# Performance work log

Measured on AMD Instinct MI355X. Metric: run time of the kernel, lower is better.

The kernel has to match this reference:

```python
import jax, jax.numpy as jnp
import numpy as np

B, L, D, K = 32, 4096, 1024, 64


def setup_inputs() -> dict:
    key = jax.random.key(0)
    k1, k2, k3, k4, k5 = jax.random.split(key, 5)
    feats = jax.random.normal(k1, (B, L, D), dtype=jnp.float32)
    assign_w = jax.random.normal(k2, (K, D), dtype=jnp.float32) * (1.0 / np.sqrt(D))
    assign_b = jax.random.normal(k3, (K,), dtype=jnp.float32) * 0.01
    centroids = jax.random.uniform(k4, (K, D), dtype=jnp.float32)
    # ensure at least one valid token per batch row (softmax over L stays finite)
    lens = jax.random.randint(k5, (B,), L // 2, L + 1, dtype=jnp.int32)
    return {"feats": feats, "lens": lens, "assign_w": assign_w,
            "assign_b": assign_b, "centroids": centroids}


def reference(feats, lens, assign_w, assign_b, centroids):
    # feats: (B,L,D); lens: (B,) int; assign_w: (K,D); assign_b: (K,); centroids: (K,D)
    Bq, Lq, Dq = feats.shape
    # padding mask; torch code slices to max(lens) first, but masked positions
    # contribute zero weight after softmax, so keeping full L is equivalent.
    mask = jnp.arange(Lq)[None, :] < lens[:, None]            # (B,L)
    logits = jnp.einsum('bld,kd->blk', feats, assign_w) + assign_b  # (B,L,K)
    logits = jnp.where(mask[:, :, None], logits, -jnp.inf)
    a = jax.nn.softmax(logits, axis=1)                         # softmax over L
    # (a[:,:,:,None] * (feats[:,:,None,:] - centroids)).sum(1) without
    # materializing the (B,L,K,D) residual tensor:
    s = a.sum(axis=1)                                          # (B,K), == 1 analytically
    vlad = jnp.einsum('blk,bld->bkd', a, feats) - s[..., None] * centroids[None]  # (B,K,D)
    out = vlad.min(axis=1)                                     # min over clusters -> (B,D)
    norm = jnp.maximum(jnp.linalg.norm(out, axis=-1, keepdims=True), 1e-12)
    return out / norm
```

## Files before the change

kernel.cpp:

```cpp
#include <hip/hip_runtime.h>
#include <math.h>

#define NB 32
#define NL 4096
#define ND 1024
#define NK 64
#define DTILE 128
#define S_SPLIT 4

typedef __bf16 bf16_t;
typedef __bf16 bf16x8 __attribute__((ext_vector_type(8)));
typedef __bf16 bf16x4 __attribute__((ext_vector_type(4)));
typedef float f32x4_t __attribute__((ext_vector_type(4)));

__global__ __launch_bounds__(256) void k_convw(const float* __restrict__ W,
                                               bf16_t* __restrict__ Wb) {
    const int i = (blockIdx.x * 256 + threadIdx.x) * 4;
    const float4 v = *(const float4*)(W + i);
    bf16x4 o;
    o[0] = (bf16_t)v.x; o[1] = (bf16_t)v.y; o[2] = (bf16_t)v.z; o[3] = (bf16_t)v.w;
    *(bf16x4*)(Wb + i) = o;
}

__global__ __launch_bounds__(256, 2) void k_logits(const float* __restrict__ feats,
                                                   const bf16_t* __restrict__ Wb,
                                                   const float* __restrict__ bias,
                                                   const int* __restrict__ lens,
                                                   float* __restrict__ logitsT,
                                                   float* __restrict__ pmax,
                                                   float* __restrict__ psum) {
    const int bid = blockIdx.x;
    const int b = bid >> 4;
    const int chunk = bid & 15;
    const int l0 = chunk << 8;
    const int len = lens[b];
    if (l0 >= len) return;
    const int t = threadIdx.x;
    const int w = t >> 6;
    const int lane = t & 63;
    const int lr = lane & 15;
    const int oct = lane >> 4;
    const int lw = l0 + w * 64;
    const float* fp = feats + ((size_t)b * NL + lw + lr) * ND + oct * 8;

    f32x4_t acc[4][4];
#pragma unroll
    for (int m = 0; m < 4; ++m)
#pragma unroll
        for (int j = 0; j < 4; ++j) acc[m][j] = (f32x4_t){0.f, 0.f, 0.f, 0.f};

#pragma unroll 2
    for (int kk = 0; kk < 32; ++kk) {
        const int d = kk * 32;
        bf16x8 af[4];
#pragma unroll
        for (int mt = 0; mt < 4; ++mt) {
            const float4 a0 = *(const float4*)(fp + (size_t)mt * 16 * ND + d);
            const float4 a1 = *(const float4*)(fp + (size_t)mt * 16 * ND + d + 4);
            af[mt][0] = (bf16_t)a0.x; af[mt][1] = (bf16_t)a0.y;
            af[mt][2] = (bf16_t)a0.z; af[mt][3] = (bf16_t)a0.w;
            af[mt][4] = (bf16_t)a1.x; af[mt][5] = (bf16_t)a1.y;
            af[mt][6] = (bf16_t)a1.z; af[mt][7] = (bf16_t)a1.w;
        }
#pragma unroll
        for (int j = 0; j < 4; ++j) {
            const bf16x8 bf = *(const bf16x8*)(Wb + (size_t)(j * 16 + lr) * ND + d + oct * 8);
#pragma unroll
            for (int mt = 0; mt < 4; ++mt)
                acc[mt][j] = __builtin_amdgcn_mfma_f32_16x16x32_bf16(af[mt], bf, acc[mt][j], 0, 0, 0);
        }
    }
    float vals[4][4][4];
#pragma unroll
    for (int mt = 0; mt < 4; ++mt)
#pragma unroll
        for (int j = 0; j < 4; ++j) {
            const int k = j * 16 + lr;
            const float bs = bias[k];
#pragma unroll
            for (int r = 0; r < 4; ++r) vals[mt][j][r] = acc[mt][j][r] + bs;
            const int lb = lw + mt * 16 + oct * 4;
            float4 st = make_float4(vals[mt][j][0], vals[mt][j][1], vals[mt][j][2], vals[mt][j][3]);
            *(float4*)(logitsT + ((size_t)b * NK + k) * NL + lb) = st;
        }
    __shared__ float red[64][17];
    __shared__ float bm[64];
    const int slot = w * 4 + oct;
#pragma unroll
    for (int j = 0; j < 4; ++j) {
        float vm = -1e30f;
#pragma unroll
        for (int mt = 0; mt < 4; ++mt) {
            const int lbase = lw + mt * 16 + oct * 4;
#pragma unroll
            for (int r = 0; r < 4; ++r)
                if (lbase + r < len) vm = fmaxf(vm, vals[mt][j][r]);
        }
        red[j * 16 + lr][slot] = vm;
    }
    __syncthreads();
    if (t < 64) {
        float m = -1e30f;
#pragma unroll
        for (int q = 0; q < 16; ++q) m = fmaxf(m, red[t][q]);
        bm[t] = m;
    }
    __syncthreads();
#pragma unroll
    for (int j = 0; j < 4; ++j) {
        const float mk = bm[j * 16 + lr];
        float sj = 0.f;
#pragma unroll
        for (int mt = 0; mt < 4; ++mt) {
            const int lbase = lw + mt * 16 + oct * 4;
#pragma unroll
            for (int r = 0; r < 4; ++r)
                if (lbase + r < len) sj += __expf(vals[mt][j][r] - mk);
        }
        red[j * 16 + lr][slot] = sj;
    }
    __syncthreads();
    if (t < 64) {
        float ssum = 0.f;
#pragma unroll
        for (int q = 0; q < 16; ++q) ssum += red[t][q];
        pmax[((size_t)b * 16 + chunk) * 64 + t] = bm[t];
        psum[((size_t)b * 16 + chunk) * 64 + t] = ssum;
    }
}

__global__ void k_sm2(const float* __restrict__ pmax, const float* __restrict__ psum,
                      const int* __restrict__ lens,
                      float* __restrict__ mbuf2) {
    const int b = blockIdx.x;
    const int k = threadIdx.x;
    const int nc = (lens[b] + 255) >> 8;
    float m = -1e30f;
    for (int c = 0; c < nc; ++c) m = fmaxf(m, pmax[((size_t)b * 16 + c) * 64 + k]);
    float s = 0.f;
    for (int c = 0; c < nc; ++c)
        s += psum[((size_t)b * 16 + c) * 64 + k] * __expf(pmax[((size_t)b * 16 + c) * 64 + k] - m);
    mbuf2[b * 64 + k] = m + logf(s);
}

__global__ __launch_bounds__(256, 3) void k_aggregate(const float* __restrict__ feats,
                                                      const float* __restrict__ logitsT,
                                                      const int* __restrict__ lens,
                                                      const float* __restrict__ mbuf2,
                                                      float* __restrict__ pO) {
    const int bid = blockIdx.x;
    const int s  = bid & 3;
    const int dc = (bid >> 2) & 7;
    const int b  = bid >> 5;
    const int d0 = dc * DTILE;
    const int t = threadIdx.x;
    const int kh = (t >> 6) & 1;
    const int dh = t >> 7;
    const int lane = t & 63;
    const int lr = lane & 15;
    const int oct = lane >> 4;
    const int len = lens[b];
    const int nT = (len + 63) >> 6;
    const int t0 = (nT * s) >> 2;
    const int t1 = (nT * (s + 1)) >> 2;

    __shared__ char fH[16 * 1024];

    const int kk0 = kh * 32 + lr;
    const float ms0 = mbuf2[b * 64 + kk0];
    const float ms1 = mbuf2[b * 64 + kk0 + 16];
    const float* lg0 = logitsT + ((size_t)b * NK + kk0) * NL;
    const float* lg1 = lg0 + (size_t)16 * NL;

    const int c4 = (t & 31) * 4;
    const int lf0 = (t >> 5) * 4;

    f32x4_t acc[2][4];
#pragma unroll
    for (int m = 0; m < 2; ++m)
#pragma unroll
        for (int n = 0; n < 4; ++n) acc[m][n] = (f32x4_t){0.f, 0.f, 0.f, 0.f};

    float4 pf[2][4];

#define LOADF(tile_)                                                                     \
    {                                                                                    \
        const int lb_ = (tile_) * 64;                                                    \
        _Pragma("unroll")                                                                \
        for (int p_ = 0; p_ < 2; ++p_) {                                                 \
            _Pragma("unroll")                                                            \
            for (int i_ = 0; i_ < 4; ++i_)                                               \
                pf[p_][i_] = *(const float4*)(feats +                                    \
                    ((size_t)b * NL + lb_ + p_ * 32 + lf0 + i_) * ND + d0 + c4);         \
        }                                                                                \
    }

    if (t0 < t1) LOADF(t0);

    for (int tile = t0; tile < t1; ++tile) {
        const int l0 = tile * 64;
        bf16x8 afH[2][2], afL[2][2];
#pragma unroll
        for (int mt = 0; mt < 2; ++mt) {
            const float* lg = mt ? lg1 : lg0;
            const float msk = mt ? ms1 : ms0;
            float4 g[4];
            g[0] = *(const float4*)(lg + l0 + oct * 8);
            g[1] = *(const float4*)(lg + l0 + oct * 8 + 4);
            g[2] = *(const float4*)(lg + l0 + 32 + oct * 8);
            g[3] = *(const float4*)(lg + l0 + 32 + oct * 8 + 4);
#pragma unroll
            for (int ks = 0; ks < 2; ++ks) {
#pragma unroll
                for (int h = 0; h < 2; ++h) {
                    const float4 v = g[ks * 2 + h];
                    const int lbase = l0 + ks * 32 + oct * 8 + h * 4;
                    float av[4];
                    av[0] = (lbase + 0 < len) ? __expf(v.x - msk) : 0.f;
                    av[1] = (lbase + 1 < len) ? __expf(v.y - msk) : 0.f;
                    av[2] = (lbase + 2 < len) ? __expf(v.z - msk) : 0.f;
                    av[3] = (lbase + 3 < len) ? __expf(v.w - msk) : 0.f;
#pragma unroll
                    for (int c = 0; c < 4; ++c) {
                        const bf16_t hi = (bf16_t)av[c];
                        afH[mt][ks][h * 4 + c] = hi;
                        afL[mt][ks][h * 4 + c] = (bf16_t)(av[c] - (float)hi);
                    }
                }
            }
        }
        __syncthreads();
#pragma unroll
        for (int p = 0; p < 2; ++p) {
            const int l4 = p * 32 + lf0;
#pragma unroll
            for (int j = 0; j < 4; ++j) {
                const int d = c4 + j;
                bf16x4 hi;
                hi[0] = (bf16_t)(&pf[p][0].x)[j];
                hi[1] = (bf16_t)(&pf[p][1].x)[j];
                hi[2] = (bf16_t)(&pf[p][2].x)[j];
                hi[3] = (bf16_t)(&pf[p][3].x)[j];
                const int chunk = (l4 >> 3) ^ ((d ^ (d >> 3)) & 7);
                const int off = d * 128 + (chunk << 4) + (l4 & 7) * 2;
                *(bf16x4*)(fH + off) = hi;
            }
        }
        if (tile + 1 < t1) LOADF(tile + 1);
        __syncthreads();
#pragma unroll
        for (int ks = 0; ks < 2; ++ks) {
            const int cbase = ks * 4 + oct;
            bf16x8 bfv[4];
#pragma unroll
            for (int n = 0; n < 4; ++n) {
                const int d = dh * 64 + n * 16 + lr;
                const int foff = d * 128 + ((cbase ^ ((d ^ (d >> 3)) & 7)) << 4);
                bfv[n] = *(const bf16x8*)(fH + foff);
            }
#pragma unroll
            for (int mt = 0; mt < 2; ++mt)
#pragma unroll
                for (int n = 0; n < 4; ++n) {
                    acc[mt][n] = __builtin_amdgcn_mfma_f32_16x16x32_bf16(afH[mt][ks], bfv[n], acc[mt][n], 0, 0, 0);
                    acc[mt][n] = __builtin_amdgcn_mfma_f32_16x16x32_bf16(afL[mt][ks], bfv[n], acc[mt][n], 0, 0, 0);
                }
        }
    }
#undef LOADF
    float* po = pO + ((size_t)((b * 8 + dc) * S_SPLIT + s)) * (NK * DTILE);
#pragma unroll
    for (int mt = 0; mt < 2; ++mt)
#pragma unroll
        for (int n = 0; n < 4; ++n) {
#pragma unroll
            for (int r = 0; r < 4; ++r) {
                const int k = kh * 32 + mt * 16 + oct * 4 + r;
                po[k * DTILE + dh * 64 + n * 16 + lr] = acc[mt][n][r];
            }
        }
}

__global__ __launch_bounds__(128) void k_combine(const float* __restrict__ pO,
                                                 const float* __restrict__ centroids,
                                                 float* __restrict__ outun) {
    const int b = blockIdx.x >> 3;
    const int d = (blockIdx.x & 7) * 128 + threadIdx.x;
    const int dc = d >> 7;
    const int dl = d & 127;
    const float* base = pO + ((size_t)(b * 8 + dc)) * S_SPLIT * NK * DTILE;
    float mn = 1e30f;
    for (int k = 0; k < NK; ++k) {
        float v = 0.f;
#pragma unroll
        for (int s = 0; s < S_SPLIT; ++s) v += base[(size_t)(s * NK + k) * DTILE + dl];
        v -= centroids[(size_t)k * ND + d];
        mn = fminf(mn, v);
    }
    outun[(size_t)b * ND + d] = mn;
}

__global__ __launch_bounds__(256) void k_norm(const float* __restrict__ outun,
                                              float* __restrict__ out) {
    const int b = blockIdx.x;
    const int t = threadIdx.x;
    float ss = 0.f;
    for (int d = t; d < ND; d += 256) {
        const float v = outun[(size_t)b * ND + d];
        ss += v * v;
    }
#pragma unroll
    for (int off = 32; off > 0; off >>= 1) ss += __shfl_down(ss, off);
    __shared__ float red[4];
    if ((t & 63) == 0) red[t >> 6] = ss;
    __syncthreads();
    const float tot = red[0] + red[1] + red[2] + red[3];
    const float inv = 1.0f / fmaxf(sqrtf(tot), 1e-12f);
    for (int d = t; d < ND; d += 256) out[(size_t)b * ND + d] = outun[(size_t)b * ND + d] * inv;
}

extern "C" void kernel_launch(void* const* d_in, const int* in_sizes, int n_in,
                              void* d_out, int out_size, void* d_ws, size_t ws_size,
                              hipStream_t stream) {
    const float* feats     = (const float*)d_in[0];
    const int*   lens      = (const int*)d_in[1];
    const float* W         = (const float*)d_in[2];
    const float* bias      = (const float*)d_in[3];
    const float* centroids = (const float*)d_in[4];
    float* out = (float*)d_out;

    char* ws = (char*)d_ws;
    size_t off = 0;
    bf16_t* Wb     = (bf16_t*)(ws + off); off += (size_t)NK * ND * sizeof(bf16_t);
    float* logitsT = (float*)(ws + off);  off += (size_t)NB * NL * NK * sizeof(float);
    float* pmax    = (float*)(ws + off);  off += (size_t)NB * 16 * NK * sizeof(float);
    float* psum    = (float*)(ws + off);  off += (size_t)NB * 16 * NK * sizeof(float);
    float* mbuf2   = (float*)(ws + off);  off += (size_t)NB * NK * sizeof(float);
    float* outun   = (float*)(ws + off);  off += (size_t)NB * ND * sizeof(float);
    float* pO      = (float*)(ws + off);

    k_convw<<<NK * ND / 1024, 256, 0, stream>>>(W, Wb);
    k_logits<<<NB * (NL / 256), 256, 0, stream>>>(feats, Wb, bias, lens, logitsT, pmax, psum);
    k_sm2<<<NB, 64, 0, stream>>>(pmax, psum, lens, mbuf2);
    k_aggregate<<<NB * 8 * S_SPLIT, 256, 0, stream>>>(feats, logitsT, lens, mbuf2, pO);
    k_combine<<<NB * 8, 128, 0, stream>>>(pO, centroids, outun);
    k_norm<<<NB, 256, 0, stream>>>(outun, out);
}
```

Before: 281.8 us.

## Widen aggregate D-tile to 256 with 512-thread blocks and prefetch logits

The aggregation kernel now covers 256 feature columns per block using 8 waves instead of 128 columns with 4 waves. This halves the number of blocks and halves how often each block re-reads and exponentiates the logits per D-chunk. Logit loads are also software-prefetched for the next tile alongside the feature prefetch, hiding their latency. In exchange the kernel uses 32KB of LDS and more registers per block, and with fewer blocks in the grid occupancy may drop.

```diff
diff --git a/kernel.cpp b/kernel.cpp
--- a/kernel.cpp
+++ b/kernel.cpp
@@ -5,7 +5,7 @@
 #define NL 4096
 #define ND 1024
 #define NK 64
-#define DTILE 128
+#define DTILE 256
 #define S_SPLIT 4
 
 typedef __bf16 bf16_t;
@@ -143,19 +143,20 @@
     mbuf2[b * 64 + k] = m + logf(s);
 }
 
-__global__ __launch_bounds__(256, 3) void k_aggregate(const float* __restrict__ feats,
+__global__ __launch_bounds__(512, 2) void k_aggregate(const float* __restrict__ feats,
                                                       const float* __restrict__ logitsT,
                                                       const int* __restrict__ lens,
                                                       const float* __restrict__ mbuf2,
                                                       float* __restrict__ pO) {
     const int bid = blockIdx.x;
     const int s  = bid & 3;
-    const int dc = (bid >> 2) & 7;
-    const int b  = bid >> 5;
+    const int dc = (bid >> 2) & 3;
+    const int b  = bid >> 4;
     const int d0 = dc * DTILE;
     const int t = threadIdx.x;
-    const int kh = (t >> 6) & 1;
-    const int dh = t >> 7;
+    const int w = t >> 6;
+    const int kh = w & 1;
+    const int dh = w >> 1;
     const int lane = t & 63;
     const int lr = lane & 15;
     const int oct = lane >> 4;
@@ -164,7 +165,7 @@
     const int t0 = (nT * s) >> 2;
     const int t1 = (nT * (s + 1)) >> 2;
 
-    __shared__ char fH[16 * 1024];
+    __shared__ char fH[32 * 1024];
 
     const int kk0 = kh * 32 + lr;
     const float ms0 = mbuf2[b * 64 + kk0];
@@ -172,8 +173,8 @@
     const float* lg0 = logitsT + ((size_t)b * NK + kk0) * NL;
     const float* lg1 = lg0 + (size_t)16 * NL;
 
-    const int c4 = (t & 31) * 4;
-    const int lf0 = (t >> 5) * 4;
+    const int c4 = (lane & 63) * 4;
+    const int r0 = w * 8;
 
     f32x4_t acc[2][4];
 #pragma unroll
@@ -181,39 +182,42 @@
 #pragma unroll
         for (int n = 0; n < 4; ++n) acc[m][n] = (f32x4_t){0.f, 0.f, 0.f, 0.f};
 
+    float4 plg[2][4];
     float4 pf[2][4];
 
-#define LOADF(tile_)                                                                     \
+#define LOADT(tile_)                                                                     \
     {                                                                                    \
         const int lb_ = (tile_) * 64;                                                    \
+        _Pragma("unroll")                                                                \
+        for (int mt_ = 0; mt_ < 2; ++mt_) {                                              \
+            const float* lg_ = mt_ ? lg1 : lg0;                                          \
+            plg[mt_][0] = *(const float4*)(lg_ + lb_ + oct * 8);                         \
+            plg[mt_][1] = *(const float4*)(lg_ + lb_ + oct * 8 + 4);                     \
+            plg[mt_][2] = *(const float4*)(lg_ + lb_ + 32 + oct * 8);                    \
+            plg[mt_][3] = *(const float4*)(lg_ + lb_ + 32 + oct * 8 + 4);                \
+        }                                                                                \
         _Pragma("unroll")                                                                \
         for (int p_ = 0; p_ < 2; ++p_) {                                                 \
             _Pragma("unroll")                                                            \
             for (int i_ = 0; i_ < 4; ++i_)                                               \
                 pf[p_][i_] = *(const float4*)(feats +                                    \
-                    ((size_t)b * NL + lb_ + p_ * 32 + lf0 + i_) * ND + d0 + c4);         \
+                    ((size_t)b * NL + lb_ + r0 + p_ * 4 + i_) * ND + d0 + c4);           \
         }                                                                                \
     }
 
-    if (t0 < t1) LOADF(t0);
+    if (t0 < t1) LOADT(t0);
 
     for (int tile = t0; tile < t1; ++tile) {
         const int l0 = tile * 64;
         bf16x8 afH[2][2], afL[2][2];
 #pragma unroll
         for (int mt = 0; mt < 2; ++mt) {
-            const float* lg = mt ? lg1 : lg0;
             const float msk = mt ? ms1 : ms0;
-            float4 g[4];
-            g[0] = *(const float4*)(lg + l0 + oct * 8);
-            g[1] = *(const float4*)(lg + l0 + oct * 8 + 4);
-            g[2] = *(const float4*)(lg + l0 + 32 + oct * 8);
-            g[3] = *(const float4*)(lg + l0 + 32 + oct * 8 + 4);
 #pragma unroll
             for (int ks = 0; ks < 2; ++ks) {
 #pragma unroll
                 for (int h = 0; h < 2; ++h) {
-                    const float4 v = g[ks * 2 + h];
+                    const float4 v = plg[mt][ks * 2 + h];
                     const int lbase = l0 + ks * 32 + oct * 8 + h * 4;
                     float av[4];
                     av[0] = (lbase + 0 < len) ? __expf(v.x - msk) : 0.f;
@@ -232,7 +236,7 @@
         __syncthreads();
 #pragma unroll
         for (int p = 0; p < 2; ++p) {
-            const int l4 = p * 32 + lf0;
+            const int l4 = r0 + p * 4;
 #pragma unroll
             for (int j = 0; j < 4; ++j) {
                 const int d = c4 + j;
@@ -246,7 +250,7 @@
                 *(bf16x4*)(fH + off) = hi;
             }
         }
-        if (tile + 1 < t1) LOADF(tile + 1);
+        if (tile + 1 < t1) LOADT(tile + 1);
         __syncthreads();
 #pragma unroll
         for (int ks = 0; ks < 2; ++ks) {
@@ -267,8 +271,8 @@
                 }
         }
     }
-#undef LOADF
-    float* po = pO + ((size_t)((b * 8 + dc) * S_SPLIT + s)) * (NK * DTILE);
+#undef LOADT
+    float* po = pO + ((size_t)((b * 4 + dc) * S_SPLIT + s)) * (NK * DTILE);
 #pragma unroll
     for (int mt = 0; mt < 2; ++mt)
 #pragma unroll
@@ -286,9 +290,9 @@
                                                  float* __restrict__ outun) {
     const int b = blockIdx.x >> 3;
     const int d = (blockIdx.x & 7) * 128 + threadIdx.x;
-    const int dc = d >> 7;
-    const int dl = d & 127;
-    const float* base = pO + ((size_t)(b * 8 + dc)) * S_SPLIT * NK * DTILE;
+    const int dc = d >> 8;
+    const int dl = d & 255;
+    const float* base = pO + ((size_t)(b * 4 + dc)) * S_SPLIT * NK * DTILE;
     float mn = 1e30f;
     for (int k = 0; k < NK; ++k) {
         float v = 0.f;
@@ -342,7 +346,7 @@
     k_convw<<<NK * ND / 1024, 256, 0, stream>>>(W, Wb);
     k_logits<<<NB * (NL / 256), 256, 0, stream>>>(feats, Wb, bias, lens, logitsT, pmax, psum);
     k_sm2<<<NB, 64, 0, stream>>>(pmax, psum, lens, mbuf2);
-    k_aggregate<<<NB * 8 * S_SPLIT, 256, 0, stream>>>(feats, logitsT, lens, mbuf2, pO);
+    k_aggregate<<<NB * 4 * S_SPLIT, 512, 0, stream>>>(feats, logitsT, lens, mbuf2, pO);
     k_combine<<<NB * 8, 128, 0, stream>>>(pO, centroids, outun);
     k_norm<<<NB, 256, 0, stream>>>(outun, out);
 }
```

Measured after the change: 287.5 us. +2.0%, slower.
